# Kernel tuning notes

Hardware: AMD Instinct MI355X
Metric: run time of the kernel (lower is better)

The kernel has to match this reference:

```python
import jax, jax.numpy as jnp
import numpy as np

B, L, C = 8, 4096, 512
KS = (3, 5, 7)
EPS = 1e-5


def _layernorm(x, g, b):
    m = jnp.mean(x, axis=-1, keepdims=True)
    v = jnp.mean((x - m) ** 2, axis=-1, keepdims=True)
    return (x - m) / jnp.sqrt(v + EPS) * g + b


def _masked_conv(x1, ids, W, bias):
    # x1: [B, C, L], ids: [B, L] int32, W: [C, C, K], bias: [C]
    K = W.shape[-1]
    pl = (K - 1) // 2
    pr = (K - 1) - pl
    xp = jnp.pad(x1, ((0, 0), (0, 0), (pl, pr)))              # [B, C, L+K-1]
    ip = jnp.pad(ids, ((0, 0), (pl, pr)), constant_values=0)  # [B, L+K-1]
    Ldim = x1.shape[-1]
    # sliding windows via K static slices (unfold equivalent)
    Xw = jnp.stack([xp[:, :, k:k + Ldim] for k in range(K)], axis=-1)   # [B, C, L, K]
    Iw = jnp.stack([ip[:, k:k + Ldim] for k in range(K)], axis=-1)      # [B, L, K]
    center = K // 2
    mask = (Iw == Iw[:, :, center:center + 1]).astype(x1.dtype)         # [B, L, K]
    out = jnp.einsum('bcik,ock->boi', Xw * mask[:, None, :, :], W)
    return out + bias[None, :, None]


def setup_inputs() -> dict:
    key = jax.random.key(0)
    ks = jax.random.split(key, 16)
    x = jax.random.normal(ks[0], (B, L, C), dtype=jnp.float32)
    # contiguous chain segments per sample (equivalent to chain_idxs ranges)
    chain_idxs = jnp.sort(jax.random.randint(ks[1], (B, L), 0, 4), axis=1).astype(jnp.int32)
    inp = {'x': x, 'chain_idxs': chain_idxs}
    for i, K in enumerate(KS):
        inp[f'conv_w{i}'] = jax.random.normal(ks[2 + i], (C, C, K), dtype=jnp.float32)
        inp[f'conv_b{i}'] = jax.random.normal(ks[5 + i], (C,), dtype=jnp.float32)
    H = 4 * C
    lim_in = float(np.sqrt(6.0 / (C + H)))
    lim_out = float(np.sqrt(6.0 / (H + C)))
    inp['mlp_w_in'] = jax.random.uniform(ks[8], (C, H), jnp.float32, -lim_in, lim_in)
    inp['mlp_b_in'] = jnp.zeros((H,), jnp.float32)
    inp['mlp_w_out'] = jax.random.uniform(ks[9], (H, C), jnp.float32, -lim_out, lim_out)
    inp['mlp_b_out'] = jnp.zeros((C,), jnp.float32)
    inp['ln1_g'] = jnp.ones((C,), jnp.float32)
    inp['ln1_b'] = jnp.zeros((C,), jnp.float32)
    inp['ln2_g'] = jnp.ones((C,), jnp.float32)
    inp['ln2_b'] = jnp.zeros((C,), jnp.float32)
    return inp


def reference(x, chain_idxs, conv_w0, conv_b0, conv_w1, conv_b1, conv_w2, conv_b2,
              mlp_w_in, mlp_b_in, mlp_w_out, mlp_b_out, ln1_g, ln1_b, ln2_g, ln2_b):
    x1 = jnp.transpose(x, (0, 2, 1))  # [B, C, L]
    for W, bias in ((conv_w0, conv_b0), (conv_w1, conv_b1), (conv_w2, conv_b2)):
        x1 = _masked_conv(x1, chain_idxs, W, bias)
    h = _layernorm(x + jnp.transpose(x1, (0, 2, 1)), ln1_g, ln1_b)
    mlp = jax.nn.gelu(h @ mlp_w_in + mlp_b_in, approximate=False) @ mlp_w_out + mlp_b_out
    out = _layernorm(h + mlp, ln2_g, ln2_b)
    return out
```

## Files before the change

### kernel.cpp

```cpp
#include <hip/hip_runtime.h>
#include <hip/hip_bf16.h>
#include <math.h>

#define B_ 8
#define L_ 4096
#define C_ 512
#define H_ 2048
#define NPOS_ (B_*L_)

typedef __attribute__((ext_vector_type(8))) short short8;
typedef __attribute__((ext_vector_type(4))) float f32x4;

__device__ __forceinline__ float bf2f(unsigned int u) {
    union { unsigned int u; float f; } c; c.u = u << 16; return c.f;
}
__device__ __forceinline__ unsigned short f2bf(float f) {
    union { float f; unsigned int u; } c; c.f = f;
    unsigned int r = c.u + 0x7fffu + ((c.u >> 16) & 1u);
    return (unsigned short)(r >> 16);
}

__device__ __forceinline__ void gload_lds16(const unsigned short* g, unsigned char* l) {
    __builtin_amdgcn_global_load_lds(
        (const __attribute__((address_space(1))) void*)g,
        (__attribute__((address_space(3))) void*)l, 16, 0, 0);
}


__global__ void __launch_bounds__(256) prep_conv_w(const float* __restrict__ W,
                                                   unsigned short* __restrict__ out, int K) {
    int idx = blockIdx.x * 256 + threadIdx.x;
    if (idx >= K * C_ * C_) return;
    int c = idx & (C_ - 1);
    int o = (idx >> 9) & (C_ - 1);
    int k = idx >> 18;
    out[idx] = f2bf(W[((size_t)o * C_ + c) * K + k]);
}

__global__ void __launch_bounds__(256) transpose_cast(const float* __restrict__ in,
                                                      unsigned short* __restrict__ out,
                                                      int R, int Cc) {
    __shared__ float tile[32][33];
    int tx = threadIdx.x & 31, ty = threadIdx.x >> 5;
    int c = blockIdx.x * 32 + tx;
    #pragma unroll
    for (int i = 0; i < 32; i += 8) {
        int r = blockIdx.y * 32 + ty + i;
        tile[ty + i][tx] = in[(size_t)r * Cc + c];
    }
    __syncthreads();
    #pragma unroll
    for (int i = 0; i < 32; i += 8) {
        int ro = blockIdx.x * 32 + ty + i;
        int co = blockIdx.y * 32 + tx;
        out[(size_t)ro * R + co] = f2bf(tile[tx][ty + i]);
    }
}

__global__ void __launch_bounds__(256) cast_f32_bf16(const float* __restrict__ in,
                                                     unsigned short* __restrict__ out, int n4) {
    int i = blockIdx.x * 256 + threadIdx.x;
    if (i >= n4) return;
    float4 v = ((const float4*)in)[i];
    uint2 o;
    o.x = (unsigned int)f2bf(v.x) | ((unsigned int)f2bf(v.y) << 16);
    o.y = (unsigned int)f2bf(v.z) | ((unsigned int)f2bf(v.w) << 16);
    ((uint2*)out)[i] = o;
}

template<int K>
__global__ void __launch_bounds__(256) conv_masked(const unsigned short* __restrict__ in,
                                                   const unsigned short* __restrict__ wt,
                                                   const float* __restrict__ bias,
                                                   const int* __restrict__ ids,
                                                   unsigned short* __restrict__ out) {
    constexpr int PL = (K - 1) / 2;
    constexpr int BM = 128, BN = 128;
    constexpr int ROWS = BM + K - 1;
    constexpr int ACH = (ROWS + 7) / 8;

    __shared__ __align__(16) unsigned char sA[ACH * 1024];
    __shared__ __align__(16) unsigned char sB[2][16 * 1024];
    __shared__ int sIds[ROWS];

    const int tid = threadIdx.x;
    const int wid = tid >> 6, lane = tid & 63;
    const int l15 = lane & 15, l4 = lane >> 4;
    const int r8 = lane >> 3, c8 = lane & 7;
    const int c16s = c8 ^ r8;
    const int i0 = blockIdx.x * BM;
    const int b = i0 >> 12;
    const int i0l = i0 & (L_ - 1);
    const int o0 = blockIdx.y * BN;
    const int wm = wid >> 1, wn = wid & 1;

    if (tid < ROWS) {
        int il = i0l + tid - PL;
        sIds[tid] = (il >= 0 && il < L_) ? ids[b * L_ + il] : -1;
    }
    __syncthreads();

    unsigned int mbits[4];
    #pragma unroll
    for (int mf = 0; mf < 4; ++mf) {
        int p = wm * 64 + mf * 16 + l15;
        int ctr = sIds[p + PL];
        unsigned int m = 0;
        #pragma unroll
        for (int k = 0; k < K; ++k)
            if (sIds[p + k] == ctr) m |= (1u << k);
        mbits[mf] = m;
    }

    f32x4 acc[4][4];
    #pragma unroll
    for (int i = 0; i < 4; ++i)
        #pragma unroll
        for (int j = 0; j < 4; ++j) acc[i][j] = 0.f;

    const short8 zero8 = 0;

    for (int cc = 0; cc < 8; ++cc) {
        #pragma unroll
        for (int it = 0; it < 5; ++it) {
            int chunk = wid + it * 4;
            if (chunk < ACH) {
                int row = chunk * 8 + r8;
                int il = i0l + row - PL;
                il = il < 0 ? 0 : (il >= L_ ? L_ - 1 : il);
                gload_lds16(in + ((size_t)(b * L_ + il) * C_ + cc * 64 + c16s * 8),
                            sA + chunk * 1024);
            }
        }
        const unsigned short* wcc = wt + (size_t)o0 * C_ + cc * 64;
        #pragma unroll
        for (int it = 0; it < 4; ++it) {
            int chunk = wid * 4 + it;
            int row = chunk * 8 + r8;
            gload_lds16(wcc + (size_t)row * C_ + c16s * 8, sB[0] + chunk * 1024);
        }
        __syncthreads();

        #pragma unroll
        for (int k = 0; k < K; ++k) {
            if (k + 1 < K) {
                const unsigned short* wkb = wcc + (size_t)(k + 1) * C_ * C_;
                #pragma unroll
                for (int it = 0; it < 4; ++it) {
                    int chunk = wid * 4 + it;
                    int row = chunk * 8 + r8;
                    gload_lds16(wkb + (size_t)row * C_ + c16s * 8,
                                sB[(k + 1) & 1] + chunk * 1024);
                }
            }
            const unsigned char* bbuf = sB[k & 1];
            #pragma unroll
            for (int kk = 0; kk < 2; ++kk) {
                short8 af[4];
                #pragma unroll
                for (int mf = 0; mf < 4; ++mf) {
                    int row = wm * 64 + mf * 16 + l15 + k;
                    int addr = (row * 128 + kk * 64 + l4 * 16) ^ ((row & 7) << 4);
                    short8 a = *(const short8*)(sA + addr);
                    af[mf] = ((mbits[mf] >> k) & 1u) ? a : zero8;
                }
                #pragma unroll
                for (int nf = 0; nf < 4; ++nf) {
                    int col = wn * 64 + nf * 16 + l15;
                    int addr = (col * 128 + kk * 64 + l4 * 16) ^ ((col & 7) << 4);
                    short8 bfr = *(const short8*)(bbuf + addr);
                    #pragma unroll
                    for (int mf = 0; mf < 4; ++mf)
                        acc[mf][nf] = __builtin_amdgcn_mfma_f32_16x16x32_bf16(af[mf], bfr, acc[mf][nf], 0, 0, 0);
                }
            }
            __syncthreads();
        }
    }

    #pragma unroll
    for (int mf = 0; mf < 4; ++mf)
        #pragma unroll
        for (int nf = 0; nf < 4; ++nf) {
            int col = o0 + wn * 64 + nf * 16 + l15;
            float bv = bias[col];
            #pragma unroll
            for (int j = 0; j < 4; ++j) {
                int p = i0 + wm * 64 + mf * 16 + l4 * 4 + j;
                out[(size_t)p * C_ + col] = f2bf(acc[mf][nf][j] + bv);
            }
        }
}


__global__ void __launch_bounds__(256) ln1_kernel(const float* __restrict__ x,
                                                  const unsigned short* __restrict__ cv,
                                                  const float* __restrict__ g,
                                                  const float* __restrict__ bb,
                                                  unsigned short* __restrict__ hb) {
    __shared__ float red[8];
    int row = blockIdx.x, t = threadIdx.x;
    size_t base = (size_t)row * C_;
    float2 xv = *(const float2*)(x + base + t * 2);
    unsigned int cu = *(const unsigned int*)(cv + base + t * 2);
    float s0 = xv.x + bf2f(cu & 0xffffu);
    float s1 = xv.y + bf2f(cu >> 16);
    float ss = s0 + s1;
    #pragma unroll
    for (int off = 32; off; off >>= 1) ss += __shfl_down(ss, off);
    if ((t & 63) == 0) red[t >> 6] = ss;
    __syncthreads();
    if (t == 0) red[4] = (red[0] + red[1] + red[2] + red[3]) * (1.f / C_);
    __syncthreads();
    float mean = red[4];
    float d0 = s0 - mean, d1 = s1 - mean;
    float vv = d0 * d0 + d1 * d1;
    #pragma unroll
    for (int off = 32; off; off >>= 1) vv += __shfl_down(vv, off);
    if ((t & 63) == 0) red[t >> 6] = vv;
    __syncthreads();
    if (t == 0) red[5] = (red[0] + red[1] + red[2] + red[3]) * (1.f / C_);
    __syncthreads();
    float rstd = rsqrtf(red[5] + 1e-5f);
    float2 gv = *(const float2*)(g + t * 2);
    float2 bv = *(const float2*)(bb + t * 2);
    float h0 = d0 * rstd * gv.x + bv.x;
    float h1 = d1 * rstd * gv.y + bv.y;
    *(unsigned int*)(hb + base + t * 2) =
        (unsigned int)f2bf(h0) | ((unsigned int)f2bf(h1) << 16);
}

__global__ void __launch_bounds__(256) ln2_bf16(const unsigned short* __restrict__ yb,
                                                const float* __restrict__ g,
                                                const float* __restrict__ bb,
                                                float* __restrict__ outp) {
    __shared__ float red[8];
    int row = blockIdx.x, t = threadIdx.x;
    size_t base = (size_t)row * C_;
    unsigned int yu = *(const unsigned int*)(yb + base + t * 2);
    float y0 = bf2f(yu & 0xffffu), y1 = bf2f(yu >> 16);
    float ss = y0 + y1;
    #pragma unroll
    for (int off = 32; off; off >>= 1) ss += __shfl_down(ss, off);
    if ((t & 63) == 0) red[t >> 6] = ss;
    __syncthreads();
    if (t == 0) red[4] = (red[0] + red[1] + red[2] + red[3]) * (1.f / C_);
    __syncthreads();
    float mean = red[4];
    float d0 = y0 - mean, d1 = y1 - mean;
    float vv = d0 * d0 + d1 * d1;
    #pragma unroll
    for (int off = 32; off; off >>= 1) vv += __shfl_down(vv, off);
    if ((t & 63) == 0) red[t >> 6] = vv;
    __syncthreads();
    if (t == 0) red[5] = (red[0] + red[1] + red[2] + red[3]) * (1.f / C_);
    __syncthreads();
    float rstd = rsqrtf(red[5] + 1e-5f);
    float2 gv = *(const float2*)(g + t * 2);
    float2 bv = *(const float2*)(bb + t * 2);
    float2 o;
    o.x = d0 * rstd * gv.x + bv.x;
    o.y = d1 * rstd * gv.y + bv.y;
    *(float2*)(outp + base + t * 2) = o;
}

template<int MODE, int BM, int BN>
__global__ void __launch_bounds__(256) gemm_bf16(const unsigned short* __restrict__ A,
                                                 const unsigned short* __restrict__ BT,
                                                 const float* __restrict__ bias,
                                                 unsigned short* __restrict__ res_io,
                                                 unsigned short* __restrict__ outp,
                                                 int Nd, int Kd) {
    constexpr int MI = BM / 32, NI = BN / 32;
    __shared__ __align__(16) unsigned char sA[BM * 128];
    __shared__ __align__(16) unsigned char sBT[BN * 128];
    const int tid = threadIdx.x;
    const int wid = tid >> 6, lane = tid & 63;
    const int l15 = lane & 15, l4 = lane >> 4;
    const int r8 = lane >> 3, c8 = lane & 7;
    const int c16s = c8 ^ r8;
    const int m0 = blockIdx.x * BM, n0 = blockIdx.y * BN;
    const int wm = wid >> 1, wn = wid & 1;

    f32x4 acc[MI][NI];
    #pragma unroll
    for (int i = 0; i < MI; ++i)
        #pragma unroll
        for (int j = 0; j < NI; ++j) acc[i][j] = 0.f;

    for (int kc = 0; kc < Kd / 64; ++kc) {
        if (kc) __syncthreads();
        const unsigned short* Ab = A + (size_t)m0 * Kd + kc * 64;
        const unsigned short* Bb = BT + (size_t)n0 * Kd + kc * 64;
        #pragma unroll
        for (int it = 0; it < BM / 32; ++it) {
            int chunk = wid * (BM / 32) + it;
            int row = chunk * 8 + r8;
            gload_lds16(Ab + (size_t)row * Kd + c16s * 8, sA + chunk * 1024);
        }
        #pragma unroll
        for (int it = 0; it < BN / 32; ++it) {
            int chunk = wid * (BN / 32) + it;
            int row = chunk * 8 + r8;
            gload_lds16(Bb + (size_t)row * Kd + c16s * 8, sBT + chunk * 1024);
        }
        __syncthreads();
        #pragma unroll
        for (int kk = 0; kk < 2; ++kk) {
            short8 af[MI], bf[NI];
            #pragma unroll
            for (int i = 0; i < MI; ++i) {
                int row = wm * (BM / 2) + i * 16 + l15;
                af[i] = *(const short8*)(sA + ((row * 128 + kk * 64 + l4 * 16) ^ ((row & 7) << 4)));
            }
            #pragma unroll
            for (int j = 0; j < NI; ++j) {
                int col = wn * (BN / 2) + j * 16 + l15;
                bf[j] = *(const short8*)(sBT + ((col * 128 + kk * 64 + l4 * 16) ^ ((col & 7) << 4)));
            }
            #pragma unroll
            for (int i = 0; i < MI; ++i)
                #pragma unroll
                for (int j = 0; j < NI; ++j)
                    acc[i][j] = __builtin_amdgcn_mfma_f32_16x16x32_bf16(af[i], bf[j], acc[i][j], 0, 0, 0);
        }
    }

    #pragma unroll
    for (int i = 0; i < MI; ++i)
        #pragma unroll
        for (int j = 0; j < NI; ++j) {
            int col = n0 + wn * (BN / 2) + j * 16 + l15;
            float bv = bias[col];
            #pragma unroll
            for (int jj = 0; jj < 4; ++jj) {
                int row = m0 + wm * (BM / 2) + i * 16 + l4 * 4 + jj;
                size_t idx = (size_t)row * Nd + col;
                float v = acc[i][j][jj] + bv;
                if (MODE == 0) {
                    v = 0.5f * v * (1.0f + erff(v * 0.70710678118654752f));
                    outp[idx] = f2bf(v);
                } else {
                    v += bf2f((unsigned int)res_io[idx]);
                    res_io[idx] = f2bf(v);
                }
            }
        }
}


extern "C" void kernel_launch(void* const* d_in, const int* in_sizes, int n_in,
                              void* d_out, int out_size, void* d_ws, size_t ws_size,
                              hipStream_t stream) {
    (void)in_sizes; (void)n_in; (void)out_size; (void)ws_size;
    const float* x    = (const float*)d_in[0];
    const int*   ids  = (const int*)d_in[1];
    const float* cw0  = (const float*)d_in[2];
    const float* cb0  = (const float*)d_in[3];
    const float* cw1  = (const float*)d_in[4];
    const float* cb1  = (const float*)d_in[5];
    const float* cw2  = (const float*)d_in[6];
    const float* cb2  = (const float*)d_in[7];
    const float* w_in = (const float*)d_in[8];
    const float* b_in = (const float*)d_in[9];
    const float* w_out= (const float*)d_in[10];
    const float* b_out= (const float*)d_in[11];
    const float* ln1g = (const float*)d_in[12];
    const float* ln1b = (const float*)d_in[13];
    const float* ln2g = (const float*)d_in[14];
    const float* ln2b = (const float*)d_in[15];

    char* ws = (char*)d_ws;
    size_t off = 0;
    auto alloc = [&](size_t bytes) { void* p = ws + off; off += (bytes + 255) & ~(size_t)255; return p; };
    unsigned short* wconv = (unsigned short*)alloc((size_t)15 * C_ * C_ * 2);
    unsigned short* wint  = (unsigned short*)alloc((size_t)H_ * C_ * 2);
    unsigned short* woutt = (unsigned short*)alloc((size_t)C_ * H_ * 2);
    unsigned short* hb    = (unsigned short*)alloc((size_t)NPOS_ * C_ * 2);
    constexpr int MCH = NPOS_ / 4;
    unsigned short* hid   = (unsigned short*)alloc((size_t)MCH * H_ * 2);

    unsigned short* act0 = (unsigned short*)d_out;
    unsigned short* act1 = act0 + (size_t)NPOS_ * C_;

    prep_conv_w<<<(3 * C_ * C_ + 255) / 256, 256, 0, stream>>>(cw0, wconv, 3);
    prep_conv_w<<<(5 * C_ * C_ + 255) / 256, 256, 0, stream>>>(cw1, wconv + (size_t)3 * C_ * C_, 5);
    prep_conv_w<<<(7 * C_ * C_ + 255) / 256, 256, 0, stream>>>(cw2, wconv + (size_t)8 * C_ * C_, 7);
    transpose_cast<<<dim3(H_ / 32, C_ / 32), 256, 0, stream>>>(w_in, wint, C_, H_);
    transpose_cast<<<dim3(C_ / 32, H_ / 32), 256, 0, stream>>>(w_out, woutt, H_, C_);
    cast_f32_bf16<<<(NPOS_ * C_ / 4 + 255) / 256, 256, 0, stream>>>(x, act0, NPOS_ * C_ / 4);

    conv_masked<3><<<dim3(NPOS_ / 128, C_ / 128), 256, 0, stream>>>(act0, wconv, cb0, ids, act1);
    conv_masked<5><<<dim3(NPOS_ / 128, C_ / 128), 256, 0, stream>>>(act1, wconv + (size_t)3 * C_ * C_, cb1, ids, act0);
    conv_masked<7><<<dim3(NPOS_ / 128, C_ / 128), 256, 0, stream>>>(act0, wconv + (size_t)8 * C_ * C_, cb2, ids, act1);

    ln1_kernel<<<NPOS_, 256, 0, stream>>>(x, act1, ln1g, ln1b, hb);

    for (int ch = 0; ch < 4; ++ch) {
        unsigned short* hbc = hb + (size_t)ch * MCH * C_;
        gemm_bf16<0, 128, 128><<<dim3(MCH / 128, H_ / 128), 256, 0, stream>>>(
            hbc, wint, b_in, nullptr, hid, H_, C_);
        gemm_bf16<1, 64, 128><<<dim3(MCH / 64, C_ / 128), 256, 0, stream>>>(
            hid, woutt, b_out, hbc, nullptr, C_, H_);
    }

    ln2_bf16<<<NPOS_, 256, 0, stream>>>(hb, ln2g, ln2b, (float*)d_out);
}
```

Before: 621.9 us.

## Double-buffer GEMM LDS tiles and use partial vmcnt waits in conv and GEMM

The GEMM kernel gets two LDS buffers for A and B tiles and prefetches the next K-chunk while computing the current one. Both the conv and GEMM loops replace the full __syncthreads (which drains all outstanding loads) with explicit s_waitcnt vmcnt(n) plus raw barriers, so the prefetch loads for the next step can stay in flight. This aims to hide global-to-LDS latency behind MFMA work. In exchange it doubles GEMM LDS use, which may lower occupancy. Correctness also relies on hand-counted vmcnt values and on raw s_barrier ordering LDS accesses without the compiler's usual waits.

```diff
diff --git a/kernel.cpp b/kernel.cpp
--- a/kernel.cpp
+++ b/kernel.cpp
@@ -10,6 +10,8 @@
 
 typedef __attribute__((ext_vector_type(8))) short short8;
 typedef __attribute__((ext_vector_type(4))) float f32x4;
+
+#define VMCNT(n) asm volatile("s_waitcnt vmcnt(" #n ")" ::: "memory")
 
 __device__ __forceinline__ float bf2f(unsigned int u) {
     union { unsigned int u; float f; } c; c.u = u << 16; return c.f;
@@ -139,7 +141,6 @@
             int row = chunk * 8 + r8;
             gload_lds16(wcc + (size_t)row * C_ + c16s * 8, sB[0] + chunk * 1024);
         }
-        __syncthreads();
 
         #pragma unroll
         for (int k = 0; k < K; ++k) {
@@ -152,7 +153,11 @@
                     gload_lds16(wkb + (size_t)row * C_ + c16s * 8,
                                 sB[(k + 1) & 1] + chunk * 1024);
                 }
-            }
+                VMCNT(4);
+            } else {
+                VMCNT(0);
+            }
+            __builtin_amdgcn_s_barrier();
             const unsigned char* bbuf = sB[k & 1];
             #pragma unroll
             for (int kk = 0; kk < 2; ++kk) {
@@ -174,7 +179,7 @@
                         acc[mf][nf] = __builtin_amdgcn_mfma_f32_16x16x32_bf16(af[mf], bfr, acc[mf][nf], 0, 0, 0);
                 }
             }
-            __syncthreads();
+            __builtin_amdgcn_s_barrier();
         }
     }
 
@@ -272,8 +277,8 @@
                                                  unsigned short* __restrict__ outp,
                                                  int Nd, int Kd) {
     constexpr int MI = BM / 32, NI = BN / 32;
-    __shared__ __align__(16) unsigned char sA[BM * 128];
-    __shared__ __align__(16) unsigned char sBT[BN * 128];
+    __shared__ __align__(16) unsigned char sA[2][BM * 128];
+    __shared__ __align__(16) unsigned char sBT[2][BN * 128];
     const int tid = threadIdx.x;
     const int wid = tid >> 6, lane = tid & 63;
     const int l15 = lane & 15, l4 = lane >> 4;
@@ -288,35 +293,47 @@
         #pragma unroll
         for (int j = 0; j < NI; ++j) acc[i][j] = 0.f;
 
-    for (int kc = 0; kc < Kd / 64; ++kc) {
-        if (kc) __syncthreads();
+    const int nk = Kd / 64;
+    auto stage = [&](int kc, int bi) {
         const unsigned short* Ab = A + (size_t)m0 * Kd + kc * 64;
         const unsigned short* Bb = BT + (size_t)n0 * Kd + kc * 64;
         #pragma unroll
-        for (int it = 0; it < BM / 32; ++it) {
-            int chunk = wid * (BM / 32) + it;
+        for (int it = 0; it < MI; ++it) {
+            int chunk = wid * MI + it;
             int row = chunk * 8 + r8;
-            gload_lds16(Ab + (size_t)row * Kd + c16s * 8, sA + chunk * 1024);
-        }
-        #pragma unroll
-        for (int it = 0; it < BN / 32; ++it) {
-            int chunk = wid * (BN / 32) + it;
+            gload_lds16(Ab + (size_t)row * Kd + c16s * 8, sA[bi] + chunk * 1024);
+        }
+        #pragma unroll
+        for (int it = 0; it < NI; ++it) {
+            int chunk = wid * NI + it;
             int row = chunk * 8 + r8;
-            gload_lds16(Bb + (size_t)row * Kd + c16s * 8, sBT + chunk * 1024);
-        }
-        __syncthreads();
+            gload_lds16(Bb + (size_t)row * Kd + c16s * 8, sBT[bi] + chunk * 1024);
+        }
+    };
+
+    stage(0, 0);
+    for (int kc = 0; kc < nk; ++kc) {
+        if (kc + 1 < nk) {
+            stage(kc + 1, (kc + 1) & 1);
+            if constexpr (MI + NI == 8) VMCNT(8); else VMCNT(6);
+        } else {
+            VMCNT(0);
+        }
+        __builtin_amdgcn_s_barrier();
+        const unsigned char* a_ = sA[kc & 1];
+        const unsigned char* b_ = sBT[kc & 1];
         #pragma unroll
         for (int kk = 0; kk < 2; ++kk) {
             short8 af[MI], bf[NI];
             #pragma unroll
             for (int i = 0; i < MI; ++i) {
                 int row = wm * (BM / 2) + i * 16 + l15;
-                af[i] = *(const short8*)(sA + ((row * 128 + kk * 64 + l4 * 16) ^ ((row & 7) << 4)));
+                af[i] = *(const short8*)(a_ + ((row * 128 + kk * 64 + l4 * 16) ^ ((row & 7) << 4)));
             }
             #pragma unroll
             for (int j = 0; j < NI; ++j) {
                 int col = wn * (BN / 2) + j * 16 + l15;
-                bf[j] = *(const short8*)(sBT + ((col * 128 + kk * 64 + l4 * 16) ^ ((col & 7) << 4)));
+                bf[j] = *(const short8*)(b_ + ((col * 128 + kk * 64 + l4 * 16) ^ ((col & 7) << 4)));
             }
             #pragma unroll
             for (int i = 0; i < MI; ++i)
@@ -324,6 +341,7 @@
                 for (int j = 0; j < NI; ++j)
                     acc[i][j] = __builtin_amdgcn_mfma_f32_16x16x32_bf16(af[i], bf[j], acc[i][j], 0, 0, 0);
         }
+        __builtin_amdgcn_s_barrier();
     }
 
     #pragma unroll
```

Result: no change. 618.8 us (-0.5%).
